# Optimization experiments

Hardware: AMD Instinct MI355X
Metric: run time of the kernel (lower is better)

The kernel has to match this reference:

```python
import jax, jax.numpy as jnp
import numpy as np

BS, N, H, W, C3D, K = 2, 4096, 64, 192, 64, 3


def _leaky(x):
    return jnp.where(x >= 0, x, 0.1 * x)


def setup_inputs() -> dict:
    key = jax.random.key(0)
    ks = jax.random.split(key, 10)
    # uv: pixel coordinates (x in [0,W), y in [0,H)), channel-first [bs,2,N]
    uv = jax.random.uniform(ks[0], (BS, 2, N), dtype=jnp.float32)
    uv = uv * jnp.array([W, H], dtype=jnp.float32)[None, :, None]
    feat_2d = jax.random.normal(ks[1], (BS, 64, H, W), dtype=jnp.float32)
    feat_3d = jax.random.normal(ks[2], (BS, C3D, N), dtype=jnp.float32)
    w1 = jax.random.normal(ks[3], (16, 3), dtype=jnp.float32) * 0.3
    b1 = jax.random.normal(ks[4], (16,), dtype=jnp.float32) * 0.1
    w2 = jax.random.normal(ks[5], (C3D, 16), dtype=jnp.float32) * 0.2
    b2 = jax.random.normal(ks[6], (C3D,), dtype=jnp.float32) * 0.1
    w_out = jax.random.normal(ks[7], (C3D, C3D), dtype=jnp.float32) * 0.1
    b_out = jax.random.normal(ks[8], (C3D,), dtype=jnp.float32) * 0.1
    return {"uv": uv, "feat_2d": feat_2d, "feat_3d": feat_3d,
            "w1": w1, "b1": b1, "w2": w2, "b2": b2,
            "w_out": w_out, "b_out": b_out}


def reference(uv, feat_2d, feat_3d, w1, b1, w2, b2, w_out, b_out):
    bs, _, image_h, image_w = feat_2d.shape
    c3d = feat_3d.shape[1]
    hw = image_h * image_w

    # mesh grid, channel order (x, y), flattened row-major over (h, w): [bs,2,HW]
    ys, xs = jnp.meshgrid(jnp.arange(image_h, dtype=jnp.float32),
                          jnp.arange(image_w, dtype=jnp.float32), indexing='ij')
    grid = jnp.stack([xs.ravel(), ys.ravel()], axis=0)  # [2, HW]
    grid = jnp.broadcast_to(grid[None], (bs, 2, hw))

    # k-NN of uv points for each grid query: squared distances [bs, HW, N]
    d2 = (jnp.sum(grid * grid, axis=1)[:, :, None]
          + jnp.sum(uv * uv, axis=1)[:, None, :]
          - 2.0 * jnp.einsum('bcq,bcn->bqn', grid, uv))
    _, knn_idx = jax.lax.top_k(-d2, K)  # [bs, HW, K]

    # gather uv and feat_3d by neighbor indices: [bs, 2+C, HW, K]
    data = jnp.concatenate([uv, feat_3d], axis=1)
    knn = jax.vmap(lambda d, i: d[:, i])(data, knn_idx)
    knn_uv, knn_feat3d = knn[:, :2], knn[:, 2:]

    knn_offset = knn_uv - grid[..., None]                      # [bs,2,HW,K]
    offset_norm = jnp.linalg.norm(knn_offset, axis=1, keepdims=True)
    score_in = jnp.concatenate([knn_offset, offset_norm], 1)   # [bs,3,HW,K]

    # score net: 1x1 conv (3->16, leaky_relu 0.1) -> 1x1 conv (16->C, sigmoid)
    h1 = _leaky(jnp.einsum('bcqk,oc->boqk', score_in, w1) + b1[None, :, None, None])
    score = jax.nn.sigmoid(jnp.einsum('bcqk,oc->boqk', h1, w2) + b2[None, :, None, None])

    final = jnp.sum(score * knn_feat3d, axis=-1)               # [bs,C,HW]
    final = final.reshape(bs, c3d, image_h, image_w)

    # out conv: 1x1 conv (C->C) + leaky_relu 0.1
    out = _leaky(jnp.einsum('bchw,oc->bohw', final, w_out) + b_out[None, :, None, None])
    return out
```

## Files before the change

kernel.cpp:

```cpp
#include <hip/hip_runtime.h>
#include <math.h>

#define NBS 2
#define NPTS 4096
#define HH 64
#define WW 192
#define HW (HH*WW)
#define NC 64
#define GX 24
#define GY 8
#define NCELL (GX*GY)

#define FBIG 3.0e38f

__global__ __launch_bounds__(256) void k0_prep(
    const float* __restrict__ uv, const float* __restrict__ f3d,
    float* __restrict__ f3dT, float4* __restrict__ binned,
    int* __restrict__ cellStart) {
#pragma clang fp contract(off)
  int bid = blockIdx.x;
  int t = threadIdx.x;
  if (bid < 128) {
    int b = bid >> 6;
    int nt = (bid & 63) << 6;
    __shared__ float tile[64][65];
    int n_in = t & 63;
    int r0 = t >> 6;
    const float* src = f3d + (size_t)b * NC * NPTS;
#pragma unroll
    for (int r = 0; r < 16; ++r) {
      int c = r0 + (r << 2);
      tile[c][n_in] = src[(size_t)c * NPTS + nt + n_in];
    }
    __syncthreads();
    float* dst = f3dT + ((size_t)b * NPTS + nt) * NC;
    int c_out = t & 63;
#pragma unroll
    for (int r = 0; r < 16; ++r) {
      int n = r0 + (r << 2);
      dst[(size_t)n * NC + c_out] = tile[c_out][n];
    }
  } else {
    int b = bid - 128;
    __shared__ int hist[NCELL + 1];
    __shared__ int cur[NCELL];
    if (t <= NCELL) hist[t] = 0;
    __syncthreads();
    const float* u0p = uv + (size_t)b * 2 * NPTS;
    const float* u1p = u0p + NPTS;
    for (int n = t; n < NPTS; n += 256) {
      float u0 = u0p[n], u1 = u1p[n];
      int cxp = min((int)(u0 * 0.125f), GX - 1);
      int cyp = min((int)(u1 * 0.125f), GY - 1);
      atomicAdd(&hist[cyp * GX + cxp + 1], 1);
    }
    __syncthreads();
    for (int off = 1; off <= NCELL; off <<= 1) {
      int v = 0;
      if (t <= NCELL && t >= off) v = hist[t - off];
      __syncthreads();
      if (t <= NCELL && t >= off) hist[t] += v;
      __syncthreads();
    }
    if (t < NCELL) cur[t] = hist[t];
    if (t <= NCELL) cellStart[b * 200 + t] = hist[t];
    __syncthreads();
    for (int n = t; n < NPTS; n += 256) {
      float u0 = u0p[n], u1 = u1p[n];
      float s0 = u0 * u0;
      float s1 = u1 * u1;
      float uu = s0 + s1;
      int cxp = min((int)(u0 * 0.125f), GX - 1);
      int cyp = min((int)(u1 * 0.125f), GY - 1);
      int pos = atomicAdd(&cur[cyp * GX + cxp], 1);
      binned[(size_t)b * NPTS + pos] =
          make_float4(u0 + u0, u1 + u1, uu, __int_as_float(n));
    }
  }
}

__global__ __launch_bounds__(256) void k_main(
    const float4* __restrict__ binned, const int* __restrict__ cellStart,
    const float* __restrict__ uv, const float* __restrict__ f3dT,
    const float* __restrict__ w1, const float* __restrict__ b1,
    const float* __restrict__ w2, const float* __restrict__ b2,
    const float* __restrict__ w_out, const float* __restrict__ b_out,
    float* __restrict__ out) {
#pragma clang fp contract(off)
  int t = threadIdx.x;
  int b = blockIdx.y;

  __shared__ int sidx[16][4];
  __shared__ float fin[16][68];

  {
    int Q = t >> 4;
    int j = t & 15;
    int qi = blockIdx.x * 16 + Q;
    int x = qi % WW, y = qi / WW;
    float xf = (float)x, yf = (float)y;
    float gg = xf * xf + yf * yf;
    int cx = x >> 3, cy = y >> 3;

    const float4* __restrict__ pts = binned + (size_t)b * NPTS;
    const int* __restrict__ cs = cellStart + b * 200;

    float v0 = FBIG, v1 = FBIG, v2 = FBIG;
    int i0 = 0x7FFFFFFF, i1 = 0x7FFFFFFF, i2 = 0x7FFFFFFF;

    auto ins = [&](float d, int gi) {
      bool lt2 = (d < v2) || (d == v2 && gi < i2);
      bool lt1 = (d < v1) || (d == v1 && gi < i1);
      bool lt0 = (d < v0) || (d == v0 && gi < i0);
      i2 = lt1 ? i1 : (lt2 ? gi : i2);
      v2 = lt1 ? v1 : (lt2 ? d : v2);
      i1 = lt0 ? i0 : (lt1 ? gi : i1);
      v1 = lt0 ? v0 : (lt1 ? d : v1);
      i0 = lt0 ? gi : i0;
      v0 = lt0 ? d : v0;
    };
    auto scanRow = [&](int ry, int cA, int cB) {
      int s = cs[ry * GX + cA];
      int e = cs[ry * GX + cB + 1];
      for (int n = s + j; n < e; n += 16) {
        float4 p = pts[n];
        float d = (gg + p.z) - __builtin_fmaf(yf, p.y, xf * p.x);
        ins(d, __float_as_int(p.w));
      }
    };
    auto mergeAll = [&]() {
#pragma unroll
      for (int m = 1; m <= 8; m <<= 1) {
        float ov0 = __shfl_xor(v0, m), ov1 = __shfl_xor(v1, m),
              ov2 = __shfl_xor(v2, m);
        int oi0 = __shfl_xor(i0, m), oi1 = __shfl_xor(i1, m),
            oi2 = __shfl_xor(i2, m);
        ins(ov0, oi0); ins(ov1, oi1); ins(ov2, oi2);
      }
    };

    int cxL = max(cx - 1, 0), cxH = min(cx + 1, GX - 1);
    int cyL = max(cy - 1, 0), cyH = min(cy + 1, GY - 1);
    for (int ry = cyL; ry <= cyH; ++ry) scanRow(ry, cxL, cxH);
    mergeAll();

    while (true) {
      bool fullDom = (cxL == 0 && cxH == GX - 1 && cyL == 0 && cyH == GY - 1);
      float dL = (cxL > 0) ? (xf - (float)(cxL * 8)) : FBIG;
      float dR = (cxH < GX - 1) ? ((float)((cxH + 1) * 8) - xf) : FBIG;
      float dB = (cyL > 0) ? (yf - (float)(cyL * 8)) : FBIG;
      float dT = (cyH < GY - 1) ? ((float)((cyH + 1) * 8) - yf) : FBIG;
      float dmin = fminf(fminf(dL, dR), fminf(dB, dT));
      if (fullDom || (v2 < dmin * dmin - 4.0f)) break;
      int nxL = max(cxL - 1, 0), nxH = min(cxH + 1, GX - 1);
      int nyL = max(cyL - 1, 0), nyH = min(cyH + 1, GY - 1);
      for (int ry = nyL; ry <= nyH; ++ry) {
        if (ry < cyL || ry > cyH) scanRow(ry, nxL, nxH);
        else {
          if (nxL < cxL) scanRow(ry, nxL, cxL - 1);
          if (nxH > cxH) scanRow(ry, cxH + 1, nxH);
        }
      }
      cxL = nxL; cxH = nxH; cyL = nyL; cyH = nyH;
      mergeAll();
    }

    if (j == 0) { sidx[Q][0] = i0; sidx[Q][1] = i1; sidx[Q][2] = i2; }
  }
  __syncthreads();

  int ql = t & 15;
  int cg = t >> 4;
  int q = blockIdx.x * 16 + ql;
  float xf = (float)(q % WW);
  float yf = (float)(q / WW);
  int idx[3] = {sidx[ql][0], sidx[ql][1], sidx[ql][2]};

  float h1a[3][16];
#pragma unroll
  for (int k = 0; k < 3; ++k) {
    int i = idx[k];
    float u0 = uv[(size_t)b * 2 * NPTS + i];
    float u1 = uv[(size_t)b * 2 * NPTS + NPTS + i];
    float dx = u0 - xf;
    float dy = u1 - yf;
    float nrm = sqrtf(__builtin_fmaf(dx, dx, dy * dy));
#pragma unroll
    for (int o = 0; o < 16; ++o) {
      float h = fmaf(w1[o * 3 + 0], dx,
               fmaf(w1[o * 3 + 1], dy,
               fmaf(w1[o * 3 + 2], nrm, b1[o])));
      h1a[k][o] = (h >= 0.0f) ? h : 0.1f * h;
    }
  }

  {
    float4 f0 = *(const float4*)(f3dT + ((size_t)b * NPTS + idx[0]) * NC + cg * 4);
    float4 f1 = *(const float4*)(f3dT + ((size_t)b * NPTS + idx[1]) * NC + cg * 4);
    float4 f2 = *(const float4*)(f3dT + ((size_t)b * NPTS + idx[2]) * NC + cg * 4);
    float fa[4] = {f0.x, f0.y, f0.z, f0.w};
    float fb[4] = {f1.x, f1.y, f1.z, f1.w};
    float fc[4] = {f2.x, f2.y, f2.z, f2.w};
#pragma unroll
    for (int cc = 0; cc < 4; ++cc) {
      int c = cg * 4 + cc;
      float bias = b2[c];
      float s0 = bias, s1 = bias, s2 = bias;
      const float4* w2r = (const float4*)(w2 + c * 16);
#pragma unroll
      for (int o4 = 0; o4 < 4; ++o4) {
        float4 wv = w2r[o4];
        float wvs[4] = {wv.x, wv.y, wv.z, wv.w};
#pragma unroll
        for (int oo = 0; oo < 4; ++oo) {
          int o = o4 * 4 + oo;
          s0 = fmaf(wvs[oo], h1a[0][o], s0);
          s1 = fmaf(wvs[oo], h1a[1][o], s1);
          s2 = fmaf(wvs[oo], h1a[2][o], s2);
        }
      }
      float g0 = 1.0f / (1.0f + __expf(-s0));
      float g1 = 1.0f / (1.0f + __expf(-s1));
      float g2 = 1.0f / (1.0f + __expf(-s2));
      fin[ql][c] = fmaf(g0, fa[cc], fmaf(g1, fb[cc], g2 * fc[cc]));
    }
  }
  __syncthreads();

  int o0 = cg * 4;
  float acc[4];
#pragma unroll
  for (int jj = 0; jj < 4; ++jj) acc[jj] = b_out[o0 + jj];
  const float4* finq = (const float4*)(&fin[ql][0]);
#pragma unroll 4
  for (int c4 = 0; c4 < 16; ++c4) {
    float4 f = finq[c4];
#pragma unroll
    for (int jj = 0; jj < 4; ++jj) {
      float4 wv = *(const float4*)(w_out + (o0 + jj) * 64 + c4 * 4);
      acc[jj] = fmaf(wv.x, f.x,
                fmaf(wv.y, f.y,
                fmaf(wv.z, f.z,
                fmaf(wv.w, f.w, acc[jj]))));
    }
  }
  float* dst = out + ((size_t)(b * 64 + o0)) * HW + q;
#pragma unroll
  for (int jj = 0; jj < 4; ++jj) {
    float v = acc[jj];
    dst[(size_t)jj * HW] = (v >= 0.0f) ? v : 0.1f * v;
  }
}

extern "C" void kernel_launch(void* const* d_in, const int* in_sizes, int n_in,
                              void* d_out, int out_size, void* d_ws, size_t ws_size,
                              hipStream_t stream) {
  const float* uv   = (const float*)d_in[0];
  const float* f3d  = (const float*)d_in[2];
  const float* w1   = (const float*)d_in[3];
  const float* b1   = (const float*)d_in[4];
  const float* w2   = (const float*)d_in[5];
  const float* b2   = (const float*)d_in[6];
  const float* wout = (const float*)d_in[7];
  const float* bout = (const float*)d_in[8];
  float* out = (float*)d_out;

  char* ws = (char*)d_ws;
  float*  f3dT      = (float*)(ws);
  float4* binned    = (float4*)(ws + 2097152);
  int*    cellStart = (int*)(ws + 2228224);

  hipLaunchKernelGGL(k0_prep, dim3(130), dim3(256), 0, stream,
                     uv, f3d, f3dT, binned, cellStart);
  hipLaunchKernelGGL(k_main, dim3(HW / 16, NBS), dim3(256), 0, stream,
                     (const float4*)binned, (const int*)cellStart,
                     uv, f3dT, w1, b1, w2, b2, wout, bout, out);
}
```

Before: 50.49 us.

## Split kNN into cell-tiled kernel staging neighbor points in LDS, separate MLP kernel

The kNN search moves into its own kernel with one block per grid cell. The 3x3 neighborhood of binned points is staged into shared memory once and shared by the cell's 64 pixels, and two waves each scan half of it. The expansion loop uses a wave-wide __all vote. The score MLP and output conv move to a second kernel that reads the kNN indices from workspace. The aim is to replace redundant per-query global scans and shuffle merges with shared-memory reuse, at the cost of an extra launch, an index round-trip through memory, and only 384 small blocks for the kNN stage.

New measurement: 64.87 us. 28.5% more time.

```diff
diff --git a/kernel.cpp b/kernel.cpp
--- a/kernel.cpp
+++ b/kernel.cpp
@@ -10,8 +10,10 @@
 #define GX 24
 #define GY 8
 #define NCELL (GX*GY)
+#define CAP 416
 
 #define FBIG 3.0e38f
+#define IBIG 0x7FFFFFFF
 
 __global__ __launch_bounds__(256) void k0_prep(
     const float* __restrict__ uv, const float* __restrict__ f3d,
@@ -20,28 +22,8 @@
 #pragma clang fp contract(off)
   int bid = blockIdx.x;
   int t = threadIdx.x;
-  if (bid < 128) {
-    int b = bid >> 6;
-    int nt = (bid & 63) << 6;
-    __shared__ float tile[64][65];
-    int n_in = t & 63;
-    int r0 = t >> 6;
-    const float* src = f3d + (size_t)b * NC * NPTS;
-#pragma unroll
-    for (int r = 0; r < 16; ++r) {
-      int c = r0 + (r << 2);
-      tile[c][n_in] = src[(size_t)c * NPTS + nt + n_in];
-    }
-    __syncthreads();
-    float* dst = f3dT + ((size_t)b * NPTS + nt) * NC;
-    int c_out = t & 63;
-#pragma unroll
-    for (int r = 0; r < 16; ++r) {
-      int n = r0 + (r << 2);
-      dst[(size_t)n * NC + c_out] = tile[c_out][n];
-    }
-  } else {
-    int b = bid - 128;
+  if (bid < 2) {
+    int b = bid;
     __shared__ int hist[NCELL + 1];
     __shared__ int cur[NCELL];
     if (t <= NCELL) hist[t] = 0;
@@ -76,74 +58,133 @@
       binned[(size_t)b * NPTS + pos] =
           make_float4(u0 + u0, u1 + u1, uu, __int_as_float(n));
     }
+  } else {
+    int bb = bid - 2;
+    int b = bb >> 6;
+    int nt = (bb & 63) << 6;
+    __shared__ float tile[64][65];
+    int n_in = t & 63;
+    int r0 = t >> 6;
+    const float* src = f3d + (size_t)b * NC * NPTS;
+#pragma unroll
+    for (int r = 0; r < 16; ++r) {
+      int c = r0 + (r << 2);
+      tile[c][n_in] = src[(size_t)c * NPTS + nt + n_in];
+    }
+    __syncthreads();
+    float* dst = f3dT + ((size_t)b * NPTS + nt) * NC;
+    int c_out = t & 63;
+#pragma unroll
+    for (int r = 0; r < 16; ++r) {
+      int n = r0 + (r << 2);
+      dst[(size_t)n * NC + c_out] = tile[c_out][n];
+    }
   }
 }
 
-__global__ __launch_bounds__(256) void k_main(
+__global__ __launch_bounds__(128) void k1_knn(
     const float4* __restrict__ binned, const int* __restrict__ cellStart,
-    const float* __restrict__ uv, const float* __restrict__ f3dT,
-    const float* __restrict__ w1, const float* __restrict__ b1,
-    const float* __restrict__ w2, const float* __restrict__ b2,
-    const float* __restrict__ w_out, const float* __restrict__ b_out,
-    float* __restrict__ out) {
+    int4* __restrict__ idxOut) {
 #pragma clang fp contract(off)
   int t = threadIdx.x;
+  int lane = t & 63;
+  int w = t >> 6;
+  int ci = blockIdx.x;
   int b = blockIdx.y;
-
-  __shared__ int sidx[16][4];
-  __shared__ float fin[16][68];
-
-  {
-    int Q = t >> 4;
-    int j = t & 15;
-    int qi = blockIdx.x * 16 + Q;
-    int x = qi % WW, y = qi / WW;
-    float xf = (float)x, yf = (float)y;
-    float gg = xf * xf + yf * yf;
-    int cx = x >> 3, cy = y >> 3;
-
-    const float4* __restrict__ pts = binned + (size_t)b * NPTS;
-    const int* __restrict__ cs = cellStart + b * 200;
-
-    float v0 = FBIG, v1 = FBIG, v2 = FBIG;
-    int i0 = 0x7FFFFFFF, i1 = 0x7FFFFFFF, i2 = 0x7FFFFFFF;
-
-    auto ins = [&](float d, int gi) {
-      bool lt2 = (d < v2) || (d == v2 && gi < i2);
-      bool lt1 = (d < v1) || (d == v1 && gi < i1);
-      bool lt0 = (d < v0) || (d == v0 && gi < i0);
-      i2 = lt1 ? i1 : (lt2 ? gi : i2);
-      v2 = lt1 ? v1 : (lt2 ? d : v2);
-      i1 = lt0 ? i0 : (lt1 ? gi : i1);
-      v1 = lt0 ? v0 : (lt1 ? d : v1);
-      i0 = lt0 ? gi : i0;
-      v0 = lt0 ? d : v0;
-    };
-    auto scanRow = [&](int ry, int cA, int cB) {
+  int cx = ci % GX, cy = ci / GX;
+  int x = cx * 8 + (lane & 7);
+  int y = cy * 8 + (lane >> 3);
+  float xf = (float)x, yf = (float)y;
+  float gg = xf * xf + yf * yf;
+
+  const float4* __restrict__ pts = binned + (size_t)b * NPTS;
+  const int* __restrict__ cs = cellStart + b * 200;
+
+  int cxL = max(cx - 1, 0), cxH = min(cx + 1, GX - 1);
+  int cyL = max(cy - 1, 0), cyH = min(cy + 1, GY - 1);
+
+  __shared__ float4 spts[CAP];
+  __shared__ float mvv[3][64];
+  __shared__ int mii[3][64];
+
+  int nrows = cyH - cyL + 1;
+  int segS[3]; int pre[4];
+  pre[0] = 0;
+#pragma unroll
+  for (int r = 0; r < 3; ++r) {
+    if (r < nrows) {
+      int s = cs[(cyL + r) * GX + cxL];
+      int e = cs[(cyL + r) * GX + cxH + 1];
+      segS[r] = s; pre[r + 1] = pre[r] + (e - s);
+    } else { segS[r] = 0; pre[r + 1] = pre[r]; }
+  }
+  int L = pre[3];
+  bool staged = (L <= CAP);
+
+  if (staged) {
+    for (int k = t; k < L; k += 128) {
+      int r = (k >= pre[1]) + (k >= pre[2]);
+      spts[k] = pts[segS[r] + (k - pre[r])];
+    }
+  }
+  __syncthreads();
+
+  float v0 = FBIG, v1 = FBIG, v2 = FBIG;
+  int i0 = IBIG, i1 = IBIG, i2 = IBIG;
+  auto ins = [&](float d, int gi) {
+    bool lt2 = (d < v2) || (d == v2 && gi < i2);
+    bool lt1 = (d < v1) || (d == v1 && gi < i1);
+    bool lt0 = (d < v0) || (d == v0 && gi < i0);
+    i2 = lt1 ? i1 : (lt2 ? gi : i2);
+    v2 = lt1 ? v1 : (lt2 ? d : v2);
+    i1 = lt0 ? i0 : (lt1 ? gi : i1);
+    v1 = lt0 ? v0 : (lt1 ? d : v1);
+    i0 = lt0 ? gi : i0;
+    v0 = lt0 ? d : v0;
+  };
+
+  if (staged) {
+    int half = (L + 1) >> 1;
+    int kB = w ? half : 0;
+    int kE = w ? L : half;
+#pragma unroll 2
+    for (int k = kB; k < kE; ++k) {
+      float4 p = spts[k];
+      float d = (gg + p.z) - __builtin_fmaf(yf, p.y, xf * p.x);
+      ins(d, __float_as_int(p.w));
+    }
+  } else {
+    for (int r = 0; r < nrows; ++r) {
+      int len = pre[r + 1] - pre[r];
+      for (int k = w; k < len; k += 2) {
+        float4 p = pts[segS[r] + k];
+        float d = (gg + p.z) - __builtin_fmaf(yf, p.y, xf * p.x);
+        ins(d, __float_as_int(p.w));
+      }
+    }
+  }
+
+  if (w == 1) {
+    mvv[0][lane] = v0; mii[0][lane] = i0;
+    mvv[1][lane] = v1; mii[1][lane] = i1;
+    mvv[2][lane] = v2; mii[2][lane] = i2;
+  }
+  __syncthreads();
+
+  if (w == 0) {
+    ins(mvv[0][lane], mii[0][lane]);
+    ins(mvv[1][lane], mii[1][lane]);
+    ins(mvv[2][lane], mii[2][lane]);
+
+    auto scanG = [&](int ry, int cA, int cB) {
       int s = cs[ry * GX + cA];
       int e = cs[ry * GX + cB + 1];
-      for (int n = s + j; n < e; n += 16) {
+      for (int n = s; n < e; ++n) {
         float4 p = pts[n];
         float d = (gg + p.z) - __builtin_fmaf(yf, p.y, xf * p.x);
         ins(d, __float_as_int(p.w));
       }
     };
-    auto mergeAll = [&]() {
-#pragma unroll
-      for (int m = 1; m <= 8; m <<= 1) {
-        float ov0 = __shfl_xor(v0, m), ov1 = __shfl_xor(v1, m),
-              ov2 = __shfl_xor(v2, m);
-        int oi0 = __shfl_xor(i0, m), oi1 = __shfl_xor(i1, m),
-            oi2 = __shfl_xor(i2, m);
-        ins(ov0, oi0); ins(ov1, oi1); ins(ov2, oi2);
-      }
-    };
-
-    int cxL = max(cx - 1, 0), cxH = min(cx + 1, GX - 1);
-    int cyL = max(cy - 1, 0), cyH = min(cy + 1, GY - 1);
-    for (int ry = cyL; ry <= cyH; ++ry) scanRow(ry, cxL, cxH);
-    mergeAll();
-
     while (true) {
       bool fullDom = (cxL == 0 && cxH == GX - 1 && cyL == 0 && cyH == GY - 1);
       float dL = (cxL > 0) ? (xf - (float)(cxL * 8)) : FBIG;
@@ -151,59 +192,73 @@
       float dB = (cyL > 0) ? (yf - (float)(cyL * 8)) : FBIG;
       float dT = (cyH < GY - 1) ? ((float)((cyH + 1) * 8) - yf) : FBIG;
       float dmin = fminf(fminf(dL, dR), fminf(dB, dT));
-      if (fullDom || (v2 < dmin * dmin - 4.0f)) break;
+      bool ok = (v2 < dmin * dmin - 4.0f);
+      if (fullDom || __all(ok)) break;
       int nxL = max(cxL - 1, 0), nxH = min(cxH + 1, GX - 1);
       int nyL = max(cyL - 1, 0), nyH = min(cyH + 1, GY - 1);
       for (int ry = nyL; ry <= nyH; ++ry) {
-        if (ry < cyL || ry > cyH) scanRow(ry, nxL, nxH);
+        if (ry < cyL || ry > cyH) scanG(ry, nxL, nxH);
         else {
-          if (nxL < cxL) scanRow(ry, nxL, cxL - 1);
-          if (nxH > cxH) scanRow(ry, cxH + 1, nxH);
+          if (nxL < cxL) scanG(ry, nxL, cxL - 1);
+          if (nxH > cxH) scanG(ry, cxH + 1, nxH);
         }
       }
       cxL = nxL; cxH = nxH; cyL = nyL; cyH = nyH;
-      mergeAll();
-    }
-
-    if (j == 0) { sidx[Q][0] = i0; sidx[Q][1] = i1; sidx[Q][2] = i2; }
-  }
-  __syncthreads();
-
-  int ql = t & 15;
-  int cg = t >> 4;
-  int q = blockIdx.x * 16 + ql;
-  float xf = (float)(q % WW);
-  float yf = (float)(q / WW);
-  int idx[3] = {sidx[ql][0], sidx[ql][1], sidx[ql][2]};
-
-  float h1a[3][16];
-#pragma unroll
-  for (int k = 0; k < 3; ++k) {
-    int i = idx[k];
-    float u0 = uv[(size_t)b * 2 * NPTS + i];
-    float u1 = uv[(size_t)b * 2 * NPTS + NPTS + i];
-    float dx = u0 - xf;
-    float dy = u1 - yf;
-    float nrm = sqrtf(__builtin_fmaf(dx, dx, dy * dy));
-#pragma unroll
-    for (int o = 0; o < 16; ++o) {
-      float h = fmaf(w1[o * 3 + 0], dx,
-               fmaf(w1[o * 3 + 1], dy,
-               fmaf(w1[o * 3 + 2], nrm, b1[o])));
-      h1a[k][o] = (h >= 0.0f) ? h : 0.1f * h;
-    }
-  }
+    }
+
+    idxOut[(size_t)b * HW + y * WW + x] = make_int4(i0, i1, i2, 0);
+  }
+}
+
+__global__ __launch_bounds__(256) void k2_mlp(
+    const int4* __restrict__ idx4, const float* __restrict__ uv,
+    const float* __restrict__ f3dT,
+    const float* __restrict__ w1, const float* __restrict__ b1,
+    const float* __restrict__ w2, const float* __restrict__ b2,
+    const float* __restrict__ w_out, const float* __restrict__ b_out,
+    float* __restrict__ out) {
+  int blk = blockIdx.x;
+  int b = blockIdx.y;
+  int t = threadIdx.x;
+
+  __shared__ float fin[16][68];
 
   {
-    float4 f0 = *(const float4*)(f3dT + ((size_t)b * NPTS + idx[0]) * NC + cg * 4);
-    float4 f1 = *(const float4*)(f3dT + ((size_t)b * NPTS + idx[1]) * NC + cg * 4);
-    float4 f2 = *(const float4*)(f3dT + ((size_t)b * NPTS + idx[2]) * NC + cg * 4);
+    int qa = t >> 4;
+    int ca = t & 15;
+    int q = blk * 16 + qa;
+    float xf = (float)(q % WW);
+    float yf = (float)(q / WW);
+    int4 id4 = idx4[(size_t)b * HW + q];
+    int idx[3] = {id4.x, id4.y, id4.z};
+
+    float h1a[3][16];
+#pragma unroll
+    for (int k = 0; k < 3; ++k) {
+      int i = idx[k];
+      float u0 = uv[(size_t)b * 2 * NPTS + i];
+      float u1 = uv[(size_t)b * 2 * NPTS + NPTS + i];
+      float dx = u0 - xf;
+      float dy = u1 - yf;
+      float nrm = sqrtf(dx * dx + dy * dy);
+#pragma unroll
+      for (int o = 0; o < 16; ++o) {
+        float h = fmaf(w1[o * 3 + 0], dx,
+                 fmaf(w1[o * 3 + 1], dy,
+                 fmaf(w1[o * 3 + 2], nrm, b1[o])));
+        h1a[k][o] = (h >= 0.0f) ? h : 0.1f * h;
+      }
+    }
+
+    float4 f0 = *(const float4*)(f3dT + ((size_t)b * NPTS + idx[0]) * NC + ca * 4);
+    float4 f1 = *(const float4*)(f3dT + ((size_t)b * NPTS + idx[1]) * NC + ca * 4);
+    float4 f2 = *(const float4*)(f3dT + ((size_t)b * NPTS + idx[2]) * NC + ca * 4);
     float fa[4] = {f0.x, f0.y, f0.z, f0.w};
     float fb[4] = {f1.x, f1.y, f1.z, f1.w};
     float fc[4] = {f2.x, f2.y, f2.z, f2.w};
 #pragma unroll
     for (int cc = 0; cc < 4; ++cc) {
-      int c = cg * 4 + cc;
+      int c = ca * 4 + cc;
       float bias = b2[c];
       float s0 = bias, s1 = bias, s2 = bias;
       const float4* w2r = (const float4*)(w2 + c * 16);
@@ -222,33 +277,38 @@
       float g0 = 1.0f / (1.0f + __expf(-s0));
       float g1 = 1.0f / (1.0f + __expf(-s1));
       float g2 = 1.0f / (1.0f + __expf(-s2));
-      fin[ql][c] = fmaf(g0, fa[cc], fmaf(g1, fb[cc], g2 * fc[cc]));
+      fin[qa][c] = fmaf(g0, fa[cc], fmaf(g1, fb[cc], g2 * fc[cc]));
     }
   }
   __syncthreads();
 
-  int o0 = cg * 4;
-  float acc[4];
-#pragma unroll
-  for (int jj = 0; jj < 4; ++jj) acc[jj] = b_out[o0 + jj];
-  const float4* finq = (const float4*)(&fin[ql][0]);
+  {
+    int qb = t & 15;
+    int cgb = t >> 4;
+    int q = blk * 16 + qb;
+    int o0 = cgb * 4;
+    float acc[4];
+#pragma unroll
+    for (int jj = 0; jj < 4; ++jj) acc[jj] = b_out[o0 + jj];
+    const float4* finq = (const float4*)(&fin[qb][0]);
 #pragma unroll 4
-  for (int c4 = 0; c4 < 16; ++c4) {
-    float4 f = finq[c4];
+    for (int c4 = 0; c4 < 16; ++c4) {
+      float4 f = finq[c4];
+#pragma unroll
+      for (int jj = 0; jj < 4; ++jj) {
+        float4 wv = *(const float4*)(w_out + (o0 + jj) * 64 + c4 * 4);
+        acc[jj] = fmaf(wv.x, f.x,
+                  fmaf(wv.y, f.y,
+                  fmaf(wv.z, f.z,
+                  fmaf(wv.w, f.w, acc[jj]))));
+      }
+    }
+    float* dst = out + ((size_t)(b * 64 + o0)) * HW + q;
 #pragma unroll
     for (int jj = 0; jj < 4; ++jj) {
-      float4 wv = *(const float4*)(w_out + (o0 + jj) * 64 + c4 * 4);
-      acc[jj] = fmaf(wv.x, f.x,
-                fmaf(wv.y, f.y,
-                fmaf(wv.z, f.z,
-                fmaf(wv.w, f.w, acc[jj]))));
-    }
-  }
-  float* dst = out + ((size_t)(b * 64 + o0)) * HW + q;
-#pragma unroll
-  for (int jj = 0; jj < 4; ++jj) {
-    float v = acc[jj];
-    dst[(size_t)jj * HW] = (v >= 0.0f) ? v : 0.1f * v;
+      float v = acc[jj];
+      dst[(size_t)jj * HW] = (v >= 0.0f) ? v : 0.1f * v;
+    }
   }
 }
 
@@ -269,10 +329,12 @@
   float*  f3dT      = (float*)(ws);
   float4* binned    = (float4*)(ws + 2097152);
   int*    cellStart = (int*)(ws + 2228224);
+  int4*   idx4      = (int4*)(ws + 2232320);
 
   hipLaunchKernelGGL(k0_prep, dim3(130), dim3(256), 0, stream,
                      uv, f3d, f3dT, binned, cellStart);
-  hipLaunchKernelGGL(k_main, dim3(HW / 16, NBS), dim3(256), 0, stream,
-                     (const float4*)binned, (const int*)cellStart,
-                     uv, f3dT, w1, b1, w2, b2, wout, bout, out);
+  hipLaunchKernelGGL(k1_knn, dim3(NCELL, NBS), dim3(128), 0, stream,
+                     (const float4*)binned, (const int*)cellStart, idx4);
+  hipLaunchKernelGGL(k2_mlp, dim3(HW / 16, NBS), dim3(256), 0, stream,
+                     (const int4*)idx4, uv, f3dT, w1, b1, w2, b2, wout, bout, out);
 }
```

## Refine spatial grid to 4-pixel cells, distribute h1 computation, split transpose blocks

Applied to the files above, without the earlier changes.

Shrinks the uniform-grid bins from 8x8 to 4x4 pixels (48x16 cells), so each k-NN query scans fewer candidate points, and replaces the block scan with a wave-level shuffle prefix sum. The first score-net layer is now computed once per (query, hidden unit) across 256 threads and staged in shared memory, instead of every channel-group thread recomputing all 48 values. The feature transpose is split into half-channel blocks so there are more blocks to run in parallel with binning, and binning blocks are ordered first. The finer grid can trigger more ring-expansion iterations for sparse regions, so a duplicate check was added to the insert step, costing extra compares.

Measured after the change: 48.11 us. 4.7% less time.

```diff
diff --git a/kernel.cpp b/kernel.cpp
--- a/kernel.cpp
+++ b/kernel.cpp
@@ -7,11 +7,13 @@
 #define WW 192
 #define HW (HH*WW)
 #define NC 64
-#define GX 24
-#define GY 8
+#define GX 48
+#define GY 16
 #define NCELL (GX*GY)
+#define CSB 1024
 
 #define FBIG 3.0e38f
+#define IBIG 0x7FFFFFFF
 
 __global__ __launch_bounds__(256) void k0_prep(
     const float* __restrict__ uv, const float* __restrict__ f3d,
@@ -20,61 +22,76 @@
 #pragma clang fp contract(off)
   int bid = blockIdx.x;
   int t = threadIdx.x;
-  if (bid < 128) {
-    int b = bid >> 6;
-    int nt = (bid & 63) << 6;
-    __shared__ float tile[64][65];
-    int n_in = t & 63;
-    int r0 = t >> 6;
-    const float* src = f3d + (size_t)b * NC * NPTS;
-#pragma unroll
-    for (int r = 0; r < 16; ++r) {
-      int c = r0 + (r << 2);
-      tile[c][n_in] = src[(size_t)c * NPTS + nt + n_in];
-    }
-    __syncthreads();
-    float* dst = f3dT + ((size_t)b * NPTS + nt) * NC;
-    int c_out = t & 63;
-#pragma unroll
-    for (int r = 0; r < 16; ++r) {
-      int n = r0 + (r << 2);
-      dst[(size_t)n * NC + c_out] = tile[c_out][n];
-    }
-  } else {
-    int b = bid - 128;
-    __shared__ int hist[NCELL + 1];
+  if (bid < 2) {
+    int b = bid;
+    __shared__ int hist[NCELL];
+    __shared__ int cum[NCELL];
     __shared__ int cur[NCELL];
-    if (t <= NCELL) hist[t] = 0;
+    for (int c = t; c < NCELL; c += 256) hist[c] = 0;
     __syncthreads();
     const float* u0p = uv + (size_t)b * 2 * NPTS;
     const float* u1p = u0p + NPTS;
     for (int n = t; n < NPTS; n += 256) {
       float u0 = u0p[n], u1 = u1p[n];
-      int cxp = min((int)(u0 * 0.125f), GX - 1);
-      int cyp = min((int)(u1 * 0.125f), GY - 1);
-      atomicAdd(&hist[cyp * GX + cxp + 1], 1);
-    }
-    __syncthreads();
-    for (int off = 1; off <= NCELL; off <<= 1) {
-      int v = 0;
-      if (t <= NCELL && t >= off) v = hist[t - off];
-      __syncthreads();
-      if (t <= NCELL && t >= off) hist[t] += v;
-      __syncthreads();
-    }
-    if (t < NCELL) cur[t] = hist[t];
-    if (t <= NCELL) cellStart[b * 200 + t] = hist[t];
+      int cxp = min((int)(u0 * 0.25f), GX - 1);
+      int cyp = min((int)(u1 * 0.25f), GY - 1);
+      atomicAdd(&hist[cyp * GX + cxp], 1);
+    }
+    __syncthreads();
+    if (t < 64) {
+      int carry = 0;
+#pragma unroll
+      for (int ck = 0; ck < NCELL / 64; ++ck) {
+        int v = hist[ck * 64 + t];
+#pragma unroll
+        for (int off = 1; off < 64; off <<= 1) {
+          int u = __shfl_up(v, off);
+          if (t >= off) v += u;
+        }
+        cum[ck * 64 + t] = v + carry;
+        carry += __shfl(v, 63);
+      }
+    }
+    __syncthreads();
+    if (t == 0) cellStart[b * CSB] = 0;
+    for (int c = t; c < NCELL; c += 256) {
+      cellStart[b * CSB + c + 1] = cum[c];
+      cur[c] = cum[c] - hist[c];
+    }
     __syncthreads();
     for (int n = t; n < NPTS; n += 256) {
       float u0 = u0p[n], u1 = u1p[n];
       float s0 = u0 * u0;
       float s1 = u1 * u1;
       float uu = s0 + s1;
-      int cxp = min((int)(u0 * 0.125f), GX - 1);
-      int cyp = min((int)(u1 * 0.125f), GY - 1);
+      int cxp = min((int)(u0 * 0.25f), GX - 1);
+      int cyp = min((int)(u1 * 0.25f), GY - 1);
       int pos = atomicAdd(&cur[cyp * GX + cxp], 1);
       binned[(size_t)b * NPTS + pos] =
           make_float4(u0 + u0, u1 + u1, uu, __int_as_float(n));
+    }
+  } else {
+    int bb = bid - 2;
+    int b = bb >> 7;
+    int half = (bb >> 6) & 1;
+    int nt = (bb & 63) << 6;
+    __shared__ float tile[32][65];
+    int n_in = t & 63;
+    int r0 = t >> 6;
+    const float* src = f3d + (size_t)b * NC * NPTS + (size_t)half * 32 * NPTS;
+#pragma unroll
+    for (int r = 0; r < 8; ++r) {
+      int c = r0 + (r << 2);
+      tile[c][n_in] = src[(size_t)c * NPTS + nt + n_in];
+    }
+    __syncthreads();
+    float* dst = f3dT + ((size_t)b * NPTS + nt) * NC + half * 32;
+    int c_out = t & 31;
+    int n0 = t >> 5;
+#pragma unroll
+    for (int r = 0; r < 8; ++r) {
+      int n = n0 + (r << 3);
+      dst[(size_t)n * NC + c_out] = tile[c_out][n];
     }
   }
 }
@@ -91,6 +108,7 @@
   int b = blockIdx.y;
 
   __shared__ int sidx[16][4];
+  __shared__ float sh1f[16 * 52];
   __shared__ float fin[16][68];
 
   {
@@ -100,18 +118,19 @@
     int x = qi % WW, y = qi / WW;
     float xf = (float)x, yf = (float)y;
     float gg = xf * xf + yf * yf;
-    int cx = x >> 3, cy = y >> 3;
+    int cx = x >> 2, cy = y >> 2;
 
     const float4* __restrict__ pts = binned + (size_t)b * NPTS;
-    const int* __restrict__ cs = cellStart + b * 200;
+    const int* __restrict__ cs = cellStart + b * CSB;
 
     float v0 = FBIG, v1 = FBIG, v2 = FBIG;
-    int i0 = 0x7FFFFFFF, i1 = 0x7FFFFFFF, i2 = 0x7FFFFFFF;
+    int i0 = IBIG, i1 = IBIG, i2 = IBIG;
 
     auto ins = [&](float d, int gi) {
-      bool lt2 = (d < v2) || (d == v2 && gi < i2);
-      bool lt1 = (d < v1) || (d == v1 && gi < i1);
-      bool lt0 = (d < v0) || (d == v0 && gi < i0);
+      bool dup = (gi == i0) || (gi == i1) || (gi == i2);
+      bool lt2 = !dup && ((d < v2) || (d == v2 && gi < i2));
+      bool lt1 = !dup && ((d < v1) || (d == v1 && gi < i1));
+      bool lt0 = !dup && ((d < v0) || (d == v0 && gi < i0));
       i2 = lt1 ? i1 : (lt2 ? gi : i2);
       v2 = lt1 ? v1 : (lt2 ? d : v2);
       i1 = lt0 ? i0 : (lt1 ? gi : i1);
@@ -146,12 +165,12 @@
 
     while (true) {
       bool fullDom = (cxL == 0 && cxH == GX - 1 && cyL == 0 && cyH == GY - 1);
-      float dL = (cxL > 0) ? (xf - (float)(cxL * 8)) : FBIG;
-      float dR = (cxH < GX - 1) ? ((float)((cxH + 1) * 8) - xf) : FBIG;
-      float dB = (cyL > 0) ? (yf - (float)(cyL * 8)) : FBIG;
-      float dT = (cyH < GY - 1) ? ((float)((cyH + 1) * 8) - yf) : FBIG;
+      float dL = (cxL > 0) ? (xf - (float)(cxL * 4)) : FBIG;
+      float dR = (cxH < GX - 1) ? ((float)((cxH + 1) * 4) - xf) : FBIG;
+      float dB = (cyL > 0) ? (yf - (float)(cyL * 4)) : FBIG;
+      float dT = (cyH < GY - 1) ? ((float)((cyH + 1) * 4) - yf) : FBIG;
       float dmin = fminf(fminf(dL, dR), fminf(dB, dT));
-      if (fullDom || (v2 < dmin * dmin - 4.0f)) break;
+      if (fullDom || (v2 < dmin * dmin - 1.0f)) break;
       int nxL = max(cxL - 1, 0), nxH = min(cxH + 1, GX - 1);
       int nyL = max(cyL - 1, 0), nyH = min(cyH + 1, GY - 1);
       for (int ry = nyL; ry <= nyH; ++ry) {
@@ -169,32 +188,43 @@
   }
   __syncthreads();
 
-  int ql = t & 15;
-  int cg = t >> 4;
-  int q = blockIdx.x * 16 + ql;
-  float xf = (float)(q % WW);
-  float yf = (float)(q / WW);
-  int idx[3] = {sidx[ql][0], sidx[ql][1], sidx[ql][2]};
-
-  float h1a[3][16];
-#pragma unroll
-  for (int k = 0; k < 3; ++k) {
-    int i = idx[k];
-    float u0 = uv[(size_t)b * 2 * NPTS + i];
-    float u1 = uv[(size_t)b * 2 * NPTS + NPTS + i];
-    float dx = u0 - xf;
-    float dy = u1 - yf;
-    float nrm = sqrtf(__builtin_fmaf(dx, dx, dy * dy));
-#pragma unroll
-    for (int o = 0; o < 16; ++o) {
-      float h = fmaf(w1[o * 3 + 0], dx,
-               fmaf(w1[o * 3 + 1], dy,
-               fmaf(w1[o * 3 + 2], nrm, b1[o])));
-      h1a[k][o] = (h >= 0.0f) ? h : 0.1f * h;
-    }
-  }
-
   {
+    int Q = t >> 4;
+    int o = t & 15;
+    int qi = blockIdx.x * 16 + Q;
+    float xf = (float)(qi % WW);
+    float yf = (float)(qi / WW);
+    float wa = w1[o * 3 + 0], wb = w1[o * 3 + 1], wc = w1[o * 3 + 2];
+    float bo = b1[o];
+#pragma unroll
+    for (int k = 0; k < 3; ++k) {
+      int i = sidx[Q][k];
+      float u0 = uv[(size_t)b * 2 * NPTS + i];
+      float u1 = uv[(size_t)b * 2 * NPTS + NPTS + i];
+      float dx = u0 - xf;
+      float dy = u1 - yf;
+      float nrm = sqrtf(__builtin_fmaf(dx, dx, dy * dy));
+      float h = fmaf(wa, dx, fmaf(wb, dy, fmaf(wc, nrm, bo)));
+      sh1f[Q * 52 + k * 16 + o] = (h >= 0.0f) ? h : 0.1f * h;
+    }
+  }
+  __syncthreads();
+
+  {
+    int ql = t & 15;
+    int cg = t >> 4;
+    float h1a[3][16];
+    {
+      const float4* h4 = (const float4*)(sh1f + ql * 52);
+#pragma unroll
+      for (int i = 0; i < 12; ++i) {
+        float4 v = h4[i];
+        int k = i >> 2, oo = (i & 3) * 4;
+        h1a[k][oo + 0] = v.x; h1a[k][oo + 1] = v.y;
+        h1a[k][oo + 2] = v.z; h1a[k][oo + 3] = v.w;
+      }
+    }
+    int idx[3] = {sidx[ql][0], sidx[ql][1], sidx[ql][2]};
     float4 f0 = *(const float4*)(f3dT + ((size_t)b * NPTS + idx[0]) * NC + cg * 4);
     float4 f1 = *(const float4*)(f3dT + ((size_t)b * NPTS + idx[1]) * NC + cg * 4);
     float4 f2 = *(const float4*)(f3dT + ((size_t)b * NPTS + idx[2]) * NC + cg * 4);
@@ -227,28 +257,33 @@
   }
   __syncthreads();
 
-  int o0 = cg * 4;
-  float acc[4];
-#pragma unroll
-  for (int jj = 0; jj < 4; ++jj) acc[jj] = b_out[o0 + jj];
-  const float4* finq = (const float4*)(&fin[ql][0]);
+  {
+    int qb = t & 15;
+    int cgb = t >> 4;
+    int q = blockIdx.x * 16 + qb;
+    int o0 = cgb * 4;
+    float acc[4];
+#pragma unroll
+    for (int jj = 0; jj < 4; ++jj) acc[jj] = b_out[o0 + jj];
+    const float4* finq = (const float4*)(&fin[qb][0]);
 #pragma unroll 4
-  for (int c4 = 0; c4 < 16; ++c4) {
-    float4 f = finq[c4];
+    for (int c4 = 0; c4 < 16; ++c4) {
+      float4 f = finq[c4];
+#pragma unroll
+      for (int jj = 0; jj < 4; ++jj) {
+        float4 wv = *(const float4*)(w_out + (o0 + jj) * 64 + c4 * 4);
+        acc[jj] = fmaf(wv.x, f.x,
+                  fmaf(wv.y, f.y,
+                  fmaf(wv.z, f.z,
+                  fmaf(wv.w, f.w, acc[jj]))));
+      }
+    }
+    float* dst = out + ((size_t)(b * 64 + o0)) * HW + q;
 #pragma unroll
     for (int jj = 0; jj < 4; ++jj) {
-      float4 wv = *(const float4*)(w_out + (o0 + jj) * 64 + c4 * 4);
-      acc[jj] = fmaf(wv.x, f.x,
-                fmaf(wv.y, f.y,
-                fmaf(wv.z, f.z,
-                fmaf(wv.w, f.w, acc[jj]))));
-    }
-  }
-  float* dst = out + ((size_t)(b * 64 + o0)) * HW + q;
-#pragma unroll
-  for (int jj = 0; jj < 4; ++jj) {
-    float v = acc[jj];
-    dst[(size_t)jj * HW] = (v >= 0.0f) ? v : 0.1f * v;
+      float v = acc[jj];
+      dst[(size_t)jj * HW] = (v >= 0.0f) ? v : 0.1f * v;
+    }
   }
 }
 
@@ -270,7 +305,7 @@
   float4* binned    = (float4*)(ws + 2097152);
   int*    cellStart = (int*)(ws + 2228224);
 
-  hipLaunchKernelGGL(k0_prep, dim3(130), dim3(256), 0, stream,
+  hipLaunchKernelGGL(k0_prep, dim3(258), dim3(256), 0, stream,
                      uv, f3d, f3dT, binned, cellStart);
   hipLaunchKernelGGL(k_main, dim3(HW / 16, NBS), dim3(256), 0, stream,
                      (const float4*)binned, (const int*)cellStart,
```
